# Kernel tuning notes

Measured on AMD Instinct MI355X. Metric: run time of the kernel, lower is better.

## Reference

```python
import jax, jax.numpy as jnp
import numpy as np

B = 16384   # batch (agents x parallel envs)
IN = 12     # input_dim
H = 64      # hidden_dim -> 2H = 128
OUT = 25    # output_dim (forced by x[:,0:5]..x[:,20:25] slicing)


def setup_inputs() -> dict:
    key = jax.random.key(0)
    ks = jax.random.split(key, 24)
    n = lambda k, s: jax.random.normal(k, s, dtype=jnp.float32)
    s = 0.1  # scale params to keep SiLU/softmax in a sane range
    return {
        "x": n(ks[0], (B, IN)),
        "na": 4,
        # mlp_in: Linear(IN, 2H) + SiLU
        "W_in": n(ks[1], (2 * H, IN)) * s, "b_in": n(ks[2], (2 * H,)) * s,
        # first attention (2H)
        "Aq4": n(ks[3], (2 * H, 2 * H)) * s, "Bq4": n(ks[4], (2 * H,)) * s,
        "Ak4": n(ks[5], (2 * H, 2 * H)) * s, "Bk4": n(ks[6], (2 * H,)) * s,
        "Av4": n(ks[7], (2 * H, 2 * H)) * s, "Bv4": n(ks[8], (2 * H,)) * s,
        # mlp_hidden_4: Linear(2H, H) + SiLU
        "W_h": n(ks[9], (H, 2 * H)) * s, "b_h": n(ks[10], (H,)) * s,
        # second attention (H)
        "Aq7": n(ks[11], (H, H)) * s, "Bq7": n(ks[12], (H,)) * s,
        "Ak7": n(ks[13], (H, H)) * s, "Bk7": n(ks[14], (H,)) * s,
        "Av7": n(ks[15], (H, H)) * s, "Bv7": n(ks[16], (H,)) * s,
        # mlp_out: Linear(H, OUT) + SiLU
        "W_out": n(ks[17], (OUT, H)) * s, "b_out": n(ks[18], (OUT,)) * s,
    }


def _attn(h, Aq, Bq, Ak, Bk, Av, Bv):
    # h: [B, D]; torch does bmm(A, x^T)+B with x of shape [B,1,D] -> seq-len-1
    # attention, i.e. scores are an outer product q k^T of shape [B, D, D].
    q = jax.nn.silu(h @ Aq.T + Bq)                      # [B, D]
    k = jax.nn.silu(h @ Ak.T + Bk)                      # [B, D]
    v = jax.nn.silu(h @ Av.T + Bv)                      # [B, D]
    a = jax.nn.softmax(q[:, :, None] * k[:, None, :], axis=2)  # [B, D, D]
    return jax.nn.silu(jnp.einsum("bij,bj->bi", a, v))  # [B, D]


def reference(x, na, W_in, b_in, Aq4, Bq4, Ak4, Bk4, Av4, Bv4,
              W_h, b_h, Aq7, Bq7, Ak7, Bk7, Av7, Bv7, W_out, b_out):
    h = jax.nn.silu(x @ W_in.T + b_in)                  # [B, 2H]
    h = _attn(h, Aq4, Bq4, Ak4, Bk4, Av4, Bv4)          # [B, 2H]
    h = jax.nn.silu(h @ W_h.T + b_h)                    # [B, H]
    h = _attn(h, Aq7, Bq7, Ak7, Bk7, Av7, Bv7)          # [B, H]
    y = jax.nn.silu(h @ W_out.T + b_out)                # [B, 25]

    # block-diagonal quadratic-form assembly (l=2, kron with ones(1,2))
    M11 = jnp.sum(y[:, 0:5] ** 2, axis=1)               # [B]
    M12 = jnp.sum(y[:, 5:10] ** 2, axis=1)
    M21 = jnp.sum(y[:, 10:15] ** 2, axis=1)
    M22 = jnp.sum(y[:, 15:20] ** 2, axis=1)
    Mpp = jnp.sum(y[:, 20:25] ** 2, axis=1)             # [B]
    q = y[:, :4]                                        # [B, 4] = [q0,q1,q2,q3]
    # M = [[diag(M11), diag(M12)],[diag(M21), diag(M22)]] (each 2x2 diag)
    quad = (M11 * (q[:, 0] ** 2 + q[:, 1] ** 2)
            + (M12 + M21) * (q[:, 0] * q[:, 2] + q[:, 1] * q[:, 3])
            + M22 * (q[:, 2] ** 2 + q[:, 3] ** 2))
    return (quad + Mpp)[:, None]                        # [B, 1]
```

## Files before the change

kernel.cpp:

```cpp
#include <hip/hip_runtime.h>

#define RPW 4
#define WAVES 4
#define RPB (RPW * WAVES)
#define NM 14

using short8 = __attribute__((ext_vector_type(8))) short;
using f32x4  = __attribute__((ext_vector_type(4))) float;

#define LOG2E 1.4426950408889634f

static __device__ __forceinline__ float ex2(float x) { return __builtin_amdgcn_exp2f(x); }
static __device__ __forceinline__ float rcpf_(float x) { return __builtin_amdgcn_rcpf(x); }
static __device__ __forceinline__ float silu_(float x) {
    return x * rcpf_(1.0f + ex2(-x * LOG2E));
}
static __device__ __forceinline__ unsigned short bfhi(float x) {
    return (unsigned short)(__float_as_uint(x) >> 16);
}
static __device__ __forceinline__ unsigned short bfrn(float x) {
    unsigned u = __float_as_uint(x);
    return (unsigned short)((u + 0x7fffu + ((u >> 16) & 1u)) >> 16);
}
static __device__ __forceinline__ float bf2f(unsigned short h) {
    return __uint_as_float(((unsigned)h) << 16);
}

template <int CTRL>
static __device__ __forceinline__ float dpp_rot(float v) {
    return __uint_as_float(
        __builtin_amdgcn_update_dpp(0u, __float_as_uint(v), CTRL, 0xF, 0xF, true));
}
static __device__ __forceinline__ float rsum16(float v) {
    v += dpp_rot<0x128>(v);
    v += dpp_rot<0x124>(v);
    v += dpp_rot<0x122>(v);
    v += dpp_rot<0x121>(v);
    return v;
}

__constant__ float c_invfact[15] = {
    1.f, 1.f, 0.5f, 1.f/6, 1.f/24, 1.f/120, 1.f/720, 1.f/5040, 1.f/40320,
    1.f/362880, 1.f/3628800, 1.f/39916800, 1.f/479001600,
    1.f/6227020800.f, 1.f/87178291200.f};

template <int O, int I>
__device__ __forceinline__ void tr(const float* __restrict__ s, float* __restrict__ d,
                                   int t0, int stride) {
    for (int idx = t0; idx < O * I; idx += stride) {
        int o = idx / I, in = idx - o * I;
        d[in * O + o] = s[idx];
    }
}

template <int TILES, int KTS, int K>
__device__ __forceinline__ void frag_cvt(const float* __restrict__ A,
                                         unsigned short* __restrict__ dst,
                                         int t0, int stride) {
    const int total = TILES * KTS * 2 * 512;
    for (int idx = t0; idx < total; idx += stride) {
        int e = idx & 7;
        int lane = (idx >> 3) & 63;
        int h = (idx >> 9) & 1;
        int kt = (idx >> 10) % KTS;
        int tile = (idx >> 10) / KTS;
        int row = tile * 16 + (lane & 15);
        int col = kt * 32 + (lane >> 4) * 8 + e;
        float a = A[row * K + col];
        unsigned short hi = bfhi(a);
        dst[idx] = h ? bfhi(a - bf2f(hi)) : hi;
    }
}

__global__ void tweights(const float* __restrict__ s0, const float* __restrict__ s1,
                         const float* __restrict__ s2, const float* __restrict__ s3,
                         const float* __restrict__ s4, const float* __restrict__ s5,
                         const float* __restrict__ s6, const float* __restrict__ s7,
                         float* __restrict__ ws) {
    const int stride = gridDim.x * blockDim.x;
    const int t0 = blockIdx.x * blockDim.x + threadIdx.x;
    tr<128, 12>(s0, ws + 0, t0, stride);
    unsigned short* u4 = (unsigned short*)(ws + 1536);
    frag_cvt<8, 4, 128>(s1, u4 + 0,     t0, stride);
    frag_cvt<8, 4, 128>(s2, u4 + 32768, t0, stride);
    frag_cvt<8, 4, 128>(s3, u4 + 65536, t0, stride);
    unsigned short* wh = (unsigned short*)(ws + 50688);
    frag_cvt<4, 4, 128>(s4, wh, t0, stride);
    unsigned short* u7 = (unsigned short*)(ws + 58880);
    frag_cvt<4, 2, 64>(s5, u7 + 0,     t0, stride);
    frag_cvt<4, 2, 64>(s6, u7 + 8192,  t0, stride);
    frag_cvt<4, 2, 64>(s7, u7 + 16384, t0, stride);
}

__global__ __launch_bounds__(256, 4) void fused_net(
    const float* __restrict__ x, const float* __restrict__ ws,
    const float* __restrict__ b_in,
    const float* __restrict__ Bq4, const float* __restrict__ Bk4, const float* __restrict__ Bv4,
    const float* __restrict__ b_h,
    const float* __restrict__ Bq7, const float* __restrict__ Bk7, const float* __restrict__ Bv7,
    const float* __restrict__ Wout, const float* __restrict__ b_out,
    float* __restrict__ out) {
    __shared__ __align__(16) unsigned short hAhi[16][136], hAlo[16][136];
    __shared__ __align__(16) unsigned short h2hi[16][80],  h2lo[16][80];
    __shared__ __align__(16) float sQ[16][132];
    __shared__ __align__(16) unsigned short sKVb[16][132][2];
    __shared__ __align__(16) float h3T[WAVES][64][RPW];
    __shared__ __align__(16) float sXT[WAVES][12][RPW];
    __shared__ __align__(16) float sY[WAVES][RPW][26];

    const int tid = threadIdx.x;
    const int w = tid >> 6;
    const int l = tid & 63;
    const int row0 = blockIdx.x * RPB + w * RPW;
    const int m16 = l & 15, quad = l >> 4;
    const int g = l & 15, r = l >> 4;
    const int R = w * RPW + r;

    const float* WinT = ws + 0;

    float bias4[6];
    #pragma unroll
    for (int t = 0; t < 6; t++) {
        const int nt = w * 6 + t;
        const int mat = nt >> 3;
        const int n = (nt & 7) * 16 + m16;
        const float* bp = (mat == 0) ? Bq4 : (mat == 1) ? Bk4 : Bv4;
        bias4[t] = bp[n];
    }
    float biasH = b_h[w * 16 + m16];
    float bias7[3];
    #pragma unroll
    for (int t = 0; t < 3; t++) {
        const int nt = w * 3 + t;
        const int mat = nt >> 2;
        const int n = (nt & 3) * 16 + m16;
        const float* bp = (mat == 0) ? Bq7 : (mat == 1) ? Bk7 : Bv7;
        bias7[t] = bp[n];
    }

    if (l < 12 * RPW) {
        float v = x[row0 * 12 + l];
        int rr = l / 12, in = l - rr * 12;
        sXT[w][in][rr] = v;
    }

    {
        float2 bb = *(const float2*)&b_in[2 * l];
        float a0[RPW], a1[RPW];
        #pragma unroll
        for (int rr = 0; rr < RPW; rr++) { a0[rr] = bb.x; a1[rr] = bb.y; }
        #pragma unroll
        for (int in = 0; in < 12; in++) {
            float2 wv = *(const float2*)&WinT[in * 128 + 2 * l];
            float4 xr = *(const float4*)&sXT[w][in][0];
            a0[0] = fmaf(xr.x, wv.x, a0[0]); a1[0] = fmaf(xr.x, wv.y, a1[0]);
            a0[1] = fmaf(xr.y, wv.x, a0[1]); a1[1] = fmaf(xr.y, wv.y, a1[1]);
            a0[2] = fmaf(xr.z, wv.x, a0[2]); a1[2] = fmaf(xr.z, wv.y, a1[2]);
            a0[3] = fmaf(xr.w, wv.x, a0[3]); a1[3] = fmaf(xr.w, wv.y, a1[3]);
        }
        #pragma unroll
        for (int rr = 0; rr < RPW; rr++) {
            float h0 = silu_(a0[rr]), h1 = silu_(a1[rr]);
            unsigned short h0h = bfhi(h0), h1h = bfhi(h1);
            float r0 = h0 - bf2f(h0h), r1 = h1 - bf2f(h1h);
            *(unsigned*)&hAhi[w * 4 + rr][2 * l] = (unsigned)h0h | ((unsigned)h1h << 16);
            *(unsigned*)&hAlo[w * 4 + rr][2 * l] = (unsigned)bfhi(r0) | ((unsigned)bfhi(r1) << 16);
        }
    }
    __syncthreads();

    {
        short8 Ah[4], Al[4];
        #pragma unroll
        for (int kt = 0; kt < 4; kt++) {
            Ah[kt] = *(const short8*)&hAhi[m16][kt * 32 + quad * 8];
            Al[kt] = *(const short8*)&hAlo[m16][kt * 32 + quad * 8];
        }
        const unsigned short* F4 = (const unsigned short*)(ws + 1536);
        short8 cb[4][2], nb[4][2];
        auto ldt = [&](int t, short8 fr[4][2]) {
            const int nt = w * 6 + t;
            const int mat = nt >> 3, tile = nt & 7;
            const unsigned short* bp = F4 + mat * 32768 + tile * 4096 + l * 8;
            #pragma unroll
            for (int kt = 0; kt < 4; kt++) {
                fr[kt][0] = *(const short8*)(bp + kt * 1024);
                fr[kt][1] = *(const short8*)(bp + kt * 1024 + 512);
            }
        };
        ldt(0, cb);
        #pragma unroll
        for (int t = 0; t < 6; t++) {
            if (t < 5) ldt(t + 1, nb);
            f32x4 acc0 = {0.f, 0.f, 0.f, 0.f};
            f32x4 acc1 = {0.f, 0.f, 0.f, 0.f};
            #pragma unroll
            for (int kt = 0; kt < 4; kt++) {
                acc0 = __builtin_amdgcn_mfma_f32_16x16x32_bf16(Ah[kt], cb[kt][0], acc0, 0, 0, 0);
                acc1 = __builtin_amdgcn_mfma_f32_16x16x32_bf16(Ah[kt], cb[kt][1], acc1, 0, 0, 0);
                acc1 = __builtin_amdgcn_mfma_f32_16x16x32_bf16(Al[kt], cb[kt][0], acc1, 0, 0, 0);
            }
            const int nt = w * 6 + t;
            const int mat = nt >> 3;
            const int n = (nt & 7) * 16 + m16;
            const float b = bias4[t];
            #pragma unroll
            for (int reg = 0; reg < 4; reg++) {
                int row = quad * 4 + reg;
                float val = silu_(b + acc0[reg] + acc1[reg]);
                if (mat == 0)      sQ[row][n] = val;
                else if (mat == 1) sKVb[row][n][0] = bfrn(val);
                else               sKVb[row][n][1] = bfrn(val);
            }
            #pragma unroll
            for (int kt = 0; kt < 4; kt++) { cb[kt][0] = nb[kt][0]; cb[kt][1] = nb[kt][1]; }
        }
    }
    __syncthreads();

    short8 whf[4][2];
    {
        const unsigned short* bp = (const unsigned short*)(ws + 50688) + w * 4096 + l * 8;
        #pragma unroll
        for (int kt = 0; kt < 4; kt++) {
            whf[kt][0] = *(const short8*)(bp + kt * 1024);
            whf[kt][1] = *(const short8*)(bp + kt * 1024 + 512);
        }
    }
    {
        float dmom[NM];
        float nmom[NM + 1];
        #pragma unroll
        for (int m = 0; m < NM; m++) dmom[m] = 0.f;
        #pragma unroll
        for (int m = 0; m <= NM; m++) nmom[m] = 0.f;
        uint4 u0 = *(const uint4*)&sKVb[R][g * 8][0];
        uint4 u1 = *(const uint4*)&sKVb[R][g * 8 + 4][0];
        unsigned us[8] = {u0.x, u0.y, u0.z, u0.w, u1.x, u1.y, u1.z, u1.w};
        #pragma unroll
        for (int jj = 0; jj < 8; jj++) {
            unsigned u = us[jj];
            float kf = __uint_as_float(u << 16);
            float vf = __uint_as_float(u & 0xffff0000u);
            nmom[0] += vf;
            float p = kf;
            dmom[0] += p; nmom[1] = fmaf(vf, p, nmom[1]);
            #pragma unroll
            for (int m = 1; m < NM; m++) {
                p *= kf;
                dmom[m] += p;
                nmom[m + 1] = fmaf(vf, p, nmom[m + 1]);
            }
        }
        #pragma unroll
        for (int m = 0; m < NM; m++) dmom[m] = rsum16(dmom[m]);
        #pragma unroll
        for (int m = 0; m <= NM; m++) nmom[m] = rsum16(nmom[m]);
        float cd[NM + 1], cn[NM + 1];
        cd[0] = 128.f; cn[0] = nmom[0];
        #pragma unroll
        for (int m = 1; m <= NM; m++) {
            cd[m] = dmom[m - 1] * c_invfact[m];
            cn[m] = nmom[m] * c_invfact[m];
        }
        float4 qa = *(const float4*)&sQ[R][g * 8];
        float4 qb = *(const float4*)&sQ[R][g * 8 + 4];
        float qs[8] = {qa.x, qa.y, qa.z, qa.w, qb.x, qb.y, qb.z, qb.w};
        unsigned hiw[4], low[4];
        #pragma unroll
        for (int i = 0; i < 8; i++) {
            float t = qs[i];
            float d = cd[NM], nn = cn[NM];
            #pragma unroll
            for (int m = NM - 1; m >= 0; m--) {
                d = fmaf(d, t, cd[m]);
                nn = fmaf(nn, t, cn[m]);
            }
            float o = silu_(nn * rcpf_(d));
            unsigned short oh = bfhi(o);
            unsigned short olo = bfhi(o - bf2f(oh));
            if (i & 1) { hiw[i >> 1] |= ((unsigned)oh) << 16; low[i >> 1] |= ((unsigned)olo) << 16; }
            else       { hiw[i >> 1] = oh; low[i >> 1] = olo; }
        }
        *(uint4*)&hAhi[R][g * 8] = make_uint4(hiw[0], hiw[1], hiw[2], hiw[3]);
        *(uint4*)&hAlo[R][g * 8] = make_uint4(low[0], low[1], low[2], low[3]);
    }
    __syncthreads();

    short8 u7f[3][2][2];
    {
        const unsigned short* U7 = (const unsigned short*)(ws + 58880);
        #pragma unroll
        for (int t = 0; t < 3; t++) {
            const int nt = w * 3 + t;
            const int mat = nt >> 2, tile = nt & 3;
            const unsigned short* bp = U7 + mat * 8192 + tile * 2048 + l * 8;
            #pragma unroll
            for (int kt = 0; kt < 2; kt++) {
                u7f[t][kt][0] = *(const short8*)(bp + kt * 1024);
                u7f[t][kt][1] = *(const short8*)(bp + kt * 1024 + 512);
            }
        }
    }
    {
        short8 Ah[4], Al[4];
        #pragma unroll
        for (int kt = 0; kt < 4; kt++) {
            Ah[kt] = *(const short8*)&hAhi[m16][kt * 32 + quad * 8];
            Al[kt] = *(const short8*)&hAlo[m16][kt * 32 + quad * 8];
        }
        const int n = w * 16 + m16;
        f32x4 acc0 = {0.f, 0.f, 0.f, 0.f};
        f32x4 acc1 = {0.f, 0.f, 0.f, 0.f};
        #pragma unroll
        for (int kt = 0; kt < 4; kt++) {
            acc0 = __builtin_amdgcn_mfma_f32_16x16x32_bf16(Ah[kt], whf[kt][0], acc0, 0, 0, 0);
            acc1 = __builtin_amdgcn_mfma_f32_16x16x32_bf16(Ah[kt], whf[kt][1], acc1, 0, 0, 0);
            acc1 = __builtin_amdgcn_mfma_f32_16x16x32_bf16(Al[kt], whf[kt][0], acc1, 0, 0, 0);
        }
        #pragma unroll
        for (int reg = 0; reg < 4; reg++) {
            int row = quad * 4 + reg;
            float hv = silu_(biasH + acc0[reg] + acc1[reg]);
            unsigned short hh = bfhi(hv);
            h2hi[row][n] = hh;
            h2lo[row][n] = bfhi(hv - bf2f(hh));
        }
    }
    __syncthreads();

    {
        short8 Ah[2], Al[2];
        #pragma unroll
        for (int kt = 0; kt < 2; kt++) {
            Ah[kt] = *(const short8*)&h2hi[m16][kt * 32 + quad * 8];
            Al[kt] = *(const short8*)&h2lo[m16][kt * 32 + quad * 8];
        }
        #pragma unroll
        for (int t = 0; t < 3; t++) {
            const int nt = w * 3 + t;
            const int mat = nt >> 2;
            const int n = (nt & 3) * 16 + m16;
            f32x4 acc0 = {0.f, 0.f, 0.f, 0.f};
            f32x4 acc1 = {0.f, 0.f, 0.f, 0.f};
            #pragma unroll
            for (int kt = 0; kt < 2; kt++) {
                acc0 = __builtin_amdgcn_mfma_f32_16x16x32_bf16(Ah[kt], u7f[t][kt][0], acc0, 0, 0, 0);
                acc1 = __builtin_amdgcn_mfma_f32_16x16x32_bf16(Ah[kt], u7f[t][kt][1], acc1, 0, 0, 0);
                acc1 = __builtin_amdgcn_mfma_f32_16x16x32_bf16(Al[kt], u7f[t][kt][0], acc1, 0, 0, 0);
            }
            const float b = bias7[t];
            #pragma unroll
            for (int reg = 0; reg < 4; reg++) {
                int row = quad * 4 + reg;
                float val = silu_(b + acc0[reg] + acc1[reg]);
                if (mat == 0)      sQ[row][n] = val;
                else if (mat == 1) sKVb[row][n][0] = bfrn(val);
                else               sKVb[row][n][1] = bfrn(val);
            }
        }
    }
    __syncthreads();

    float4 wq[8];
    float bb7;
    {
        const int o_ = l & 31;
        const int half_ = l >> 5;
        const int oc_ = (o_ < 25) ? o_ : 0;
        const float* wp = Wout + oc_ * 64 + half_ * 32;
        #pragma unroll
        for (int q = 0; q < 8; q++) wq[q] = *(const float4*)&wp[4 * q];
        bb7 = (half_ == 0) ? b_out[oc_] : 0.f;
    }
    {
        float dmom[NM];
        float nmom[NM + 1];
        #pragma unroll
        for (int m = 0; m < NM; m++) dmom[m] = 0.f;
        #pragma unroll
        for (int m = 0; m <= NM; m++) nmom[m] = 0.f;
        uint2 u0 = *(const uint2*)&sKVb[R][g * 4][0];
        uint2 u1 = *(const uint2*)&sKVb[R][g * 4 + 2][0];
        unsigned us[4] = {u0.x, u0.y, u1.x, u1.y};
        #pragma unroll
        for (int jj = 0; jj < 4; jj++) {
            unsigned u = us[jj];
            float kf = __uint_as_float(u << 16);
            float vf = __uint_as_float(u & 0xffff0000u);
            nmom[0] += vf;
            float p = kf;
            dmom[0] += p; nmom[1] = fmaf(vf, p, nmom[1]);
            #pragma unroll
            for (int m = 1; m < NM; m++) {
                p *= kf;
                dmom[m] += p;
                nmom[m + 1] = fmaf(vf, p, nmom[m + 1]);
            }
        }
        #pragma unroll
        for (int m = 0; m < NM; m++) dmom[m] = rsum16(dmom[m]);
        #pragma unroll
        for (int m = 0; m <= NM; m++) nmom[m] = rsum16(nmom[m]);
        float cd[NM + 1], cn[NM + 1];
        cd[0] = 64.f; cn[0] = nmom[0];
        #pragma unroll
        for (int m = 1; m <= NM; m++) {
            cd[m] = dmom[m - 1] * c_invfact[m];
            cn[m] = nmom[m] * c_invfact[m];
        }
        float4 qa = *(const float4*)&sQ[R][g * 4];
        float qs[4] = {qa.x, qa.y, qa.z, qa.w};
        #pragma unroll
        for (int i = 0; i < 4; i++) {
            float t = qs[i];
            float d = cd[NM], nn = cn[NM];
            #pragma unroll
            for (int m = NM - 1; m >= 0; m--) {
                d = fmaf(d, t, cd[m]);
                nn = fmaf(nn, t, cn[m]);
            }
            h3T[w][g * 4 + i][r] = silu_(nn * rcpf_(d));
        }
    }

    {
        const int half = l >> 5;
        float y[RPW];
        #pragma unroll
        for (int rr = 0; rr < RPW; rr++) y[rr] = bb7;
        const int in0 = half * 32;
        #pragma unroll
        for (int q = 0; q < 8; q++) {
            float wa[4] = {wq[q].x, wq[q].y, wq[q].z, wq[q].w};
            #pragma unroll
            for (int ii = 0; ii < 4; ii++) {
                int in = in0 + 4 * q + ii;
                float4 xr = *(const float4*)&h3T[w][in][0];
                y[0] = fmaf(xr.x, wa[ii], y[0]);
                y[1] = fmaf(xr.y, wa[ii], y[1]);
                y[2] = fmaf(xr.z, wa[ii], y[2]);
                y[3] = fmaf(xr.w, wa[ii], y[3]);
            }
        }
        #pragma unroll
        for (int rr = 0; rr < RPW; rr++) {
            float full = y[rr] + __shfl_xor(y[rr], 32, 64);
            if (l < 25) sY[w][rr][l] = silu_(full);
        }
    }

    if (l < RPW) {
        const int rr = l;
        float y[25];
        #pragma unroll
        for (int c = 0; c < 25; c++) y[c] = sY[w][rr][c];
        float M11 = 0.f, M12 = 0.f, M21 = 0.f, M22 = 0.f, Mpp = 0.f;
        #pragma unroll
        for (int c = 0; c < 5; c++) {
            M11 = fmaf(y[c], y[c], M11);
            M12 = fmaf(y[5 + c], y[5 + c], M12);
            M21 = fmaf(y[10 + c], y[10 + c], M21);
            M22 = fmaf(y[15 + c], y[15 + c], M22);
            Mpp = fmaf(y[20 + c], y[20 + c], Mpp);
        }
        float quad = M11 * (y[0] * y[0] + y[1] * y[1])
                   + (M12 + M21) * (y[0] * y[2] + y[1] * y[3])
                   + M22 * (y[2] * y[2] + y[3] * y[3]);
        out[row0 + rr] = quad + Mpp;
    }
}

extern "C" void kernel_launch(void* const* d_in, const int* in_sizes, int n_in,
                              void* d_out, int out_size, void* d_ws, size_t ws_size,
                              hipStream_t stream) {
    const float* x    = (const float*)d_in[0];
    const float* W_in = (const float*)d_in[2];
    const float* b_in = (const float*)d_in[3];
    const float* Aq4  = (const float*)d_in[4];
    const float* Bq4  = (const float*)d_in[5];
    const float* Ak4  = (const float*)d_in[6];
    const float* Bk4  = (const float*)d_in[7];
    const float* Av4  = (const float*)d_in[8];
    const float* Bv4  = (const float*)d_in[9];
    const float* W_h  = (const float*)d_in[10];
    const float* b_h  = (const float*)d_in[11];
    const float* Aq7  = (const float*)d_in[12];
    const float* Bq7  = (const float*)d_in[13];
    const float* Ak7  = (const float*)d_in[14];
    const float* Bk7  = (const float*)d_in[15];
    const float* Av7  = (const float*)d_in[16];
    const float* Bv7  = (const float*)d_in[17];
    const float* Wout = (const float*)d_in[18];
    const float* bout = (const float*)d_in[19];
    float* ws = (float*)d_ws;

    tweights<<<256, 256, 0, stream>>>(W_in, Aq4, Ak4, Av4, W_h, Aq7, Ak7, Av7, ws);

    const int B = in_sizes[0] / 12;
    const int grid = B / RPB;
    fused_net<<<grid, 256, 0, stream>>>(x, ws, b_in, Bq4, Bk4, Bv4,
                                        b_h, Bq7, Bk7, Bv7, Wout, bout, (float*)d_out);
}
```

Before: 132.6 us.

## Split block into two 8-row half-batches and interleave MFMA and moment phases

Each 16-row block is split into two independent 8-row sub-batches (A and B) with separate shared buffers. The schedule is software-pipelined so one sub-batch's MFMA projections run interleaved with the other's VALU-heavy Taylor-moment softmax and epilogue, using 32-lane reductions. The aim is to overlap matrix-core work with vector ALU work inside a wave. In exchange, each MFMA now uses only 8 of its 16 rows, doubling MFMA issue per row, and shared memory use and register pressure go up.

```diff
diff --git a/kernel.cpp b/kernel.cpp
--- a/kernel.cpp
+++ b/kernel.cpp
@@ -1,8 +1,6 @@
 #include <hip/hip_runtime.h>
 
-#define RPW 4
-#define WAVES 4
-#define RPB (RPW * WAVES)
+#define RPB 16
 #define NM 14
 
 using short8 = __attribute__((ext_vector_type(8))) short;
@@ -38,6 +36,12 @@
     v += dpp_rot<0x121>(v);
     return v;
 }
+static __device__ __forceinline__ float rsum32(float v) {
+    v = rsum16(v);
+    v += __uint_as_float(
+        (unsigned)__builtin_amdgcn_ds_swizzle((int)__float_as_uint(v), 0x401F));
+    return v;
+}
 
 __constant__ float c_invfact[15] = {
     1.f, 1.f, 0.5f, 1.f/6, 1.f/24, 1.f/120, 1.f/720, 1.f/5040, 1.f/40320,
@@ -52,7 +56,6 @@
         d[in * O + o] = s[idx];
     }
 }
-
 template <int TILES, int KTS, int K>
 __device__ __forceinline__ void frag_cvt(const float* __restrict__ A,
                                          unsigned short* __restrict__ dst,
@@ -92,6 +95,288 @@
     frag_cvt<4, 2, 64>(s7, u7 + 16384, t0, stride);
 }
 
+
+#define STAGE_X(S, OFF) \
+    if (l < 24) { \
+        float v = x[(base + (OFF) + w * 2) * 12 + l]; \
+        int rr = l / 12, in = l - rr * 12; \
+        sXT##S[w][in][rr] = v; \
+    }
+
+#define PH1(S) { \
+    float2 bb = *(const float2*)&b_in[2 * l]; \
+    float a0[2], a1[2]; \
+    a0[0] = bb.x; a0[1] = bb.x; a1[0] = bb.y; a1[1] = bb.y; \
+    _Pragma("unroll") \
+    for (int in = 0; in < 12; in++) { \
+        float2 wv = *(const float2*)&WinT[in * 128 + 2 * l]; \
+        float2 xr = *(const float2*)&sXT##S[w][in][0]; \
+        a0[0] = fmaf(xr.x, wv.x, a0[0]); a1[0] = fmaf(xr.x, wv.y, a1[0]); \
+        a0[1] = fmaf(xr.y, wv.x, a0[1]); a1[1] = fmaf(xr.y, wv.y, a1[1]); \
+    } \
+    _Pragma("unroll") \
+    for (int rr = 0; rr < 2; rr++) { \
+        float h0 = silu_(a0[rr]), h1 = silu_(a1[rr]); \
+        unsigned short h0h = bfhi(h0), h1h = bfhi(h1); \
+        float r0 = h0 - bf2f(h0h), r1 = h1 - bf2f(h1h); \
+        *(unsigned*)&hAhi##S[w * 2 + rr][2 * l] = (unsigned)h0h | ((unsigned)h1h << 16); \
+        *(unsigned*)&hAlo##S[w * 2 + rr][2 * l] = (unsigned)bfhi(r0) | ((unsigned)bfhi(r1) << 16); \
+    } }
+
+#define LDA4(S) \
+    short8 Ah##S[4], Al##S[4]; \
+    _Pragma("unroll") \
+    for (int kt = 0; kt < 4; kt++) { \
+        Ah##S[kt] = *(const short8*)&hAhi##S[m8][kt * 32 + quad * 8]; \
+        Al##S[kt] = *(const short8*)&hAlo##S[m8][kt * 32 + quad * 8]; \
+    }
+
+#define TILE4(S, T) { \
+    const int nt = w * 6 + (T); \
+    const int mat = nt >> 3; \
+    const int n = (nt & 7) * 16 + m16; \
+    const unsigned short* bp = F4 + mat * 32768 + (nt & 7) * 4096 + l * 8; \
+    f32x4 acc0 = {0.f, 0.f, 0.f, 0.f}; \
+    f32x4 acc1 = {0.f, 0.f, 0.f, 0.f}; \
+    _Pragma("unroll") \
+    for (int kt = 0; kt < 4; kt++) { \
+        short8 bh = *(const short8*)(bp + kt * 1024); \
+        short8 bl = *(const short8*)(bp + kt * 1024 + 512); \
+        acc0 = __builtin_amdgcn_mfma_f32_16x16x32_bf16(Ah##S[kt], bh, acc0, 0, 0, 0); \
+        acc1 = __builtin_amdgcn_mfma_f32_16x16x32_bf16(Ah##S[kt], bl, acc1, 0, 0, 0); \
+        acc1 = __builtin_amdgcn_mfma_f32_16x16x32_bf16(Al##S[kt], bh, acc1, 0, 0, 0); \
+    } \
+    const float bv = bias4[(T)]; \
+    if (quad < 2) { \
+        _Pragma("unroll") \
+        for (int reg = 0; reg < 4; reg++) { \
+            int row = quad * 4 + reg; \
+            float val = silu_(bv + acc0[reg] + acc1[reg]); \
+            if (mat == 0)      sQ##S[row][n] = val; \
+            else if (mat == 1) sKV##S[row][n][0] = bfrn(val); \
+            else               sKV##S[row][n][1] = bfrn(val); \
+        } \
+    } }
+
+#define P3_STATE(S) \
+    const int row3 = w * 2 + r32; \
+    uint4 u3 = *(const uint4*)&sKV##S[row3][g32 * 4][0]; \
+    float dm[NM], nm[NM + 1];
+
+#define P3_MOM(S) { \
+    _Pragma("unroll") for (int m = 0; m < NM; m++) dm[m] = 0.f; \
+    _Pragma("unroll") for (int m = 0; m <= NM; m++) nm[m] = 0.f; \
+    unsigned usv[4] = {u3.x, u3.y, u3.z, u3.w}; \
+    _Pragma("unroll") \
+    for (int jj = 0; jj < 4; jj++) { \
+        unsigned u = usv[jj]; \
+        float kf = __uint_as_float(u << 16); \
+        float vf = __uint_as_float(u & 0xffff0000u); \
+        nm[0] += vf; \
+        float p = kf; \
+        dm[0] += p; nm[1] = fmaf(vf, p, nm[1]); \
+        _Pragma("unroll") \
+        for (int m = 1; m < NM; m++) { \
+            p *= kf; \
+            dm[m] += p; \
+            nm[m + 1] = fmaf(vf, p, nm[m + 1]); \
+        } \
+    } }
+
+#define P3_REDD() \
+    _Pragma("unroll") for (int m = 0; m < NM; m++) dm[m] = rsum32(dm[m]);
+#define P3_REDN() \
+    _Pragma("unroll") for (int m = 0; m <= NM; m++) nm[m] = rsum32(nm[m]);
+
+#define P3_HORN(S) { \
+    float cd[NM + 1], cn[NM + 1]; \
+    cd[0] = 128.f; cn[0] = nm[0]; \
+    _Pragma("unroll") \
+    for (int m = 1; m <= NM; m++) { \
+        cd[m] = dm[m - 1] * c_invfact[m]; \
+        cn[m] = nm[m] * c_invfact[m]; \
+    } \
+    float4 qa = *(const float4*)&sQ##S[row3][g32 * 4]; \
+    float qs[4] = {qa.x, qa.y, qa.z, qa.w}; \
+    unsigned hiw[2], low[2]; \
+    _Pragma("unroll") \
+    for (int i = 0; i < 4; i++) { \
+        float t = qs[i]; \
+        float d = cd[NM], nn = cn[NM]; \
+        _Pragma("unroll") \
+        for (int m = NM - 1; m >= 0; m--) { \
+            d = fmaf(d, t, cd[m]); \
+            nn = fmaf(nn, t, cn[m]); \
+        } \
+        float o = silu_(nn * rcpf_(d)); \
+        unsigned short oh = bfhi(o); \
+        unsigned short olo = bfhi(o - bf2f(oh)); \
+        if (i & 1) { hiw[i >> 1] |= ((unsigned)oh) << 16; low[i >> 1] |= ((unsigned)olo) << 16; } \
+        else       { hiw[i >> 1] = oh; low[i >> 1] = olo; } \
+    } \
+    *(uint2*)&hAhi##S[row3][g32 * 4] = make_uint2(hiw[0], hiw[1]); \
+    *(uint2*)&hAlo##S[row3][g32 * 4] = make_uint2(low[0], low[1]); }
+
+#define P4_MFMA(S) \
+    short8 Ah4[4], Al4[4]; \
+    _Pragma("unroll") \
+    for (int kt = 0; kt < 4; kt++) { \
+        Ah4[kt] = *(const short8*)&hAhi##S[m8][kt * 32 + quad * 8]; \
+        Al4[kt] = *(const short8*)&hAlo##S[m8][kt * 32 + quad * 8]; \
+    } \
+    const unsigned short* bp4 = WH + w * 4096 + l * 8; \
+    f32x4 p40 = {0.f, 0.f, 0.f, 0.f}; \
+    f32x4 p41 = {0.f, 0.f, 0.f, 0.f}; \
+    _Pragma("unroll") \
+    for (int kt = 0; kt < 4; kt++) { \
+        short8 bh = *(const short8*)(bp4 + kt * 1024); \
+        short8 bl = *(const short8*)(bp4 + kt * 1024 + 512); \
+        p40 = __builtin_amdgcn_mfma_f32_16x16x32_bf16(Ah4[kt], bh, p40, 0, 0, 0); \
+        p41 = __builtin_amdgcn_mfma_f32_16x16x32_bf16(Ah4[kt], bl, p41, 0, 0, 0); \
+        p41 = __builtin_amdgcn_mfma_f32_16x16x32_bf16(Al4[kt], bh, p41, 0, 0, 0); \
+    }
+
+#define P4_EPI(S) { \
+    const int n4 = w * 16 + m16; \
+    if (quad < 2) { \
+        _Pragma("unroll") \
+        for (int reg = 0; reg < 4; reg++) { \
+            int row = quad * 4 + reg; \
+            float hv = silu_(biasH + p40[reg] + p41[reg]); \
+            unsigned short hh = bfhi(hv); \
+            h2hi##S[row][n4] = hh; \
+            h2lo##S[row][n4] = bfhi(hv - bf2f(hh)); \
+        } \
+    } }
+
+#define LDA2(S) \
+    short8 Ah2##S[2], Al2##S[2]; \
+    _Pragma("unroll") \
+    for (int kt = 0; kt < 2; kt++) { \
+        Ah2##S[kt] = *(const short8*)&h2hi##S[m8][kt * 32 + quad * 8]; \
+        Al2##S[kt] = *(const short8*)&h2lo##S[m8][kt * 32 + quad * 8]; \
+    }
+
+#define TILE7(S, T) { \
+    const int nt = w * 3 + (T); \
+    const int mat = nt >> 2; \
+    const int n = (nt & 3) * 16 + m16; \
+    const unsigned short* bp = U7 + mat * 8192 + (nt & 3) * 2048 + l * 8; \
+    f32x4 acc0 = {0.f, 0.f, 0.f, 0.f}; \
+    f32x4 acc1 = {0.f, 0.f, 0.f, 0.f}; \
+    _Pragma("unroll") \
+    for (int kt = 0; kt < 2; kt++) { \
+        short8 bh = *(const short8*)(bp + kt * 1024); \
+        short8 bl = *(const short8*)(bp + kt * 1024 + 512); \
+        acc0 = __builtin_amdgcn_mfma_f32_16x16x32_bf16(Ah2##S[kt], bh, acc0, 0, 0, 0); \
+        acc1 = __builtin_amdgcn_mfma_f32_16x16x32_bf16(Ah2##S[kt], bl, acc1, 0, 0, 0); \
+        acc1 = __builtin_amdgcn_mfma_f32_16x16x32_bf16(Al2##S[kt], bh, acc1, 0, 0, 0); \
+    } \
+    const float bv = bias7[(T)]; \
+    if (quad < 2) { \
+        _Pragma("unroll") \
+        for (int reg = 0; reg < 4; reg++) { \
+            int row = quad * 4 + reg; \
+            float val = silu_(bv + acc0[reg] + acc1[reg]); \
+            if (mat == 0)      sQ##S[row][n] = val; \
+            else if (mat == 1) sKV##S[row][n][0] = bfrn(val); \
+            else               sKV##S[row][n][1] = bfrn(val); \
+        } \
+    } }
+
+#define P6_STATE(S) \
+    const int row6 = w * 2 + r32; \
+    uint2 u6 = *(const uint2*)&sKV##S[row6][g32 * 2][0]; \
+    float dm6[NM], nm6[NM + 1];
+
+#define P6_MOM(S) { \
+    _Pragma("unroll") for (int m = 0; m < NM; m++) dm6[m] = 0.f; \
+    _Pragma("unroll") for (int m = 0; m <= NM; m++) nm6[m] = 0.f; \
+    unsigned usv[2] = {u6.x, u6.y}; \
+    _Pragma("unroll") \
+    for (int jj = 0; jj < 2; jj++) { \
+        unsigned u = usv[jj]; \
+        float kf = __uint_as_float(u << 16); \
+        float vf = __uint_as_float(u & 0xffff0000u); \
+        nm6[0] += vf; \
+        float p = kf; \
+        dm6[0] += p; nm6[1] = fmaf(vf, p, nm6[1]); \
+        _Pragma("unroll") \
+        for (int m = 1; m < NM; m++) { \
+            p *= kf; \
+            dm6[m] += p; \
+            nm6[m + 1] = fmaf(vf, p, nm6[m + 1]); \
+        } \
+    } }
+
+#define P6_RED() \
+    _Pragma("unroll") for (int m = 0; m < NM; m++) dm6[m] = rsum32(dm6[m]); \
+    _Pragma("unroll") for (int m = 0; m <= NM; m++) nm6[m] = rsum32(nm6[m]);
+
+#define P6_HORN(S) { \
+    float cd[NM + 1], cn[NM + 1]; \
+    cd[0] = 64.f; cn[0] = nm6[0]; \
+    _Pragma("unroll") \
+    for (int m = 1; m <= NM; m++) { \
+        cd[m] = dm6[m - 1] * c_invfact[m]; \
+        cn[m] = nm6[m] * c_invfact[m]; \
+    } \
+    float2 qa = *(const float2*)&sQ##S[row6][g32 * 2]; \
+    float qs[2] = {qa.x, qa.y}; \
+    _Pragma("unroll") \
+    for (int i = 0; i < 2; i++) { \
+        float t = qs[i]; \
+        float d = cd[NM], nn = cn[NM]; \
+        _Pragma("unroll") \
+        for (int m = NM - 1; m >= 0; m--) { \
+            d = fmaf(d, t, cd[m]); \
+            nn = fmaf(nn, t, cn[m]); \
+        } \
+        h3T##S[w][g32 * 2 + i][r32] = silu_(nn * rcpf_(d)); \
+    } }
+
+#define P7(S) { \
+    const int o_ = l & 31; \
+    const int half_ = l >> 5; \
+    const int oc_ = (o_ < 25) ? o_ : 0; \
+    float bb7 = (half_ == 0) ? b_out[oc_] : 0.f; \
+    float y0 = bb7, y1 = bb7; \
+    const int in0 = half_ * 32; \
+    const float* wp = Wout + oc_ * 64 + in0; \
+    _Pragma("unroll") \
+    for (int q8 = 0; q8 < 8; q8++) { \
+        float4 wq4 = *(const float4*)&wp[4 * q8]; \
+        float wa[4] = {wq4.x, wq4.y, wq4.z, wq4.w}; \
+        _Pragma("unroll") \
+        for (int ii = 0; ii < 4; ii++) { \
+            float2 xr = *(const float2*)&h3T##S[w][in0 + 4 * q8 + ii][0]; \
+            y0 = fmaf(xr.x, wa[ii], y0); \
+            y1 = fmaf(xr.y, wa[ii], y1); \
+        } \
+    } \
+    float f0 = y0 + __shfl_xor(y0, 32, 64); \
+    float f1 = y1 + __shfl_xor(y1, 32, 64); \
+    if (l < 25) { sY##S[w][0][l] = silu_(f0); sY##S[w][1][l] = silu_(f1); } }
+
+#define P8(S, OFF) \
+    if (l < 2) { \
+        float yv[25]; \
+        _Pragma("unroll") for (int c = 0; c < 25; c++) yv[c] = sY##S[w][l][c]; \
+        float M11 = 0.f, M12 = 0.f, M21 = 0.f, M22 = 0.f, Mpp = 0.f; \
+        _Pragma("unroll") \
+        for (int c = 0; c < 5; c++) { \
+            M11 = fmaf(yv[c], yv[c], M11); \
+            M12 = fmaf(yv[5 + c], yv[5 + c], M12); \
+            M21 = fmaf(yv[10 + c], yv[10 + c], M21); \
+            M22 = fmaf(yv[15 + c], yv[15 + c], M22); \
+            Mpp = fmaf(yv[20 + c], yv[20 + c], Mpp); \
+        } \
+        float qf = M11 * (yv[0] * yv[0] + yv[1] * yv[1]) \
+                 + (M12 + M21) * (yv[0] * yv[2] + yv[1] * yv[3]) \
+                 + M22 * (yv[2] * yv[2] + yv[3] * yv[3]); \
+        out[base + (OFF) + w * 2 + l] = qf + Mpp; \
+    }
+
 __global__ __launch_bounds__(256, 4) void fused_net(
     const float* __restrict__ x, const float* __restrict__ ws,
     const float* __restrict__ b_in,
@@ -100,23 +385,28 @@
     const float* __restrict__ Bq7, const float* __restrict__ Bk7, const float* __restrict__ Bv7,
     const float* __restrict__ Wout, const float* __restrict__ b_out,
     float* __restrict__ out) {
-    __shared__ __align__(16) unsigned short hAhi[16][136], hAlo[16][136];
-    __shared__ __align__(16) unsigned short h2hi[16][80],  h2lo[16][80];
-    __shared__ __align__(16) float sQ[16][132];
-    __shared__ __align__(16) unsigned short sKVb[16][132][2];
-    __shared__ __align__(16) float h3T[WAVES][64][RPW];
-    __shared__ __align__(16) float sXT[WAVES][12][RPW];
-    __shared__ __align__(16) float sY[WAVES][RPW][26];
+    __shared__ __align__(16) unsigned short hAhiA[8][136], hAloA[8][136];
+    __shared__ __align__(16) unsigned short hAhiB[8][136], hAloB[8][136];
+    __shared__ __align__(16) unsigned short h2hiA[8][80],  h2loA[8][80];
+    __shared__ __align__(16) unsigned short h2hiB[8][80],  h2loB[8][80];
+    __shared__ __align__(16) float sQA[8][132], sQB[8][132];
+    __shared__ __align__(16) unsigned short sKVA[8][132][2], sKVB[8][132][2];
+    __shared__ __align__(16) float h3TA[4][64][2], h3TB[4][64][2];
+    __shared__ __align__(16) float sXTA[4][12][2], sXTB[4][12][2];
+    __shared__ __align__(16) float sYA[4][2][26], sYB[4][2][26];
 
     const int tid = threadIdx.x;
     const int w = tid >> 6;
     const int l = tid & 63;
-    const int row0 = blockIdx.x * RPB + w * RPW;
+    const int base = blockIdx.x * RPB;
     const int m16 = l & 15, quad = l >> 4;
-    const int g = l & 15, r = l >> 4;
-    const int R = w * RPW + r;
+    const int m8 = m16 & 7;
+    const int g32 = l & 31, r32 = l >> 5;
 
     const float* WinT = ws + 0;
+    const unsigned short* F4 = (const unsigned short*)(ws + 1536);
+    const unsigned short* WH = (const unsigned short*)(ws + 50688);
+    const unsigned short* U7 = (const unsigned short*)(ws + 58880);
 
     float bias4[6];
     #pragma unroll
@@ -138,337 +428,83 @@
         bias7[t] = bp[n];
     }
 
-    if (l < 12 * RPW) {
-        float v = x[row0 * 12 + l];
-        int rr = l / 12, in = l - rr * 12;
-        sXT[w][in][rr] = v;
-    }
+    STAGE_X(A, 0)
+    STAGE_X(B, 8)
+    PH1(A)
+    __syncthreads();
 
     {
-        float2 bb = *(const float2*)&b_in[2 * l];
-        float a0[RPW], a1[RPW];
-        #pragma unroll
-        for (int rr = 0; rr < RPW; rr++) { a0[rr] = bb.x; a1[rr] = bb.y; }
-        #pragma unroll
-        for (int in = 0; in < 12; in++) {
-            float2 wv = *(const float2*)&WinT[in * 128 + 2 * l];
-            float4 xr = *(const float4*)&sXT[w][in][0];
-            a0[0] = fmaf(xr.x, wv.x, a0[0]); a1[0] = fmaf(xr.x, wv.y, a1[0]);
-            a0[1] = fmaf(xr.y, wv.x, a0[1]); a1[1] = fmaf(xr.y, wv.y, a1[1]);
-            a0[2] = fmaf(xr.z, wv.x, a0[2]); a1[2] = fmaf(xr.z, wv.y, a1[2]);
-            a0[3] = fmaf(xr.w, wv.x, a0[3]); a1[3] = fmaf(xr.w, wv.y, a1[3]);
-        }
-        #pragma unroll
-        for (int rr = 0; rr < RPW; rr++) {
-            float h0 = silu_(a0[rr]), h1 = silu_(a1[rr]);
-            unsigned short h0h = bfhi(h0), h1h = bfhi(h1);
-            float r0 = h0 - bf2f(h0h), r1 = h1 - bf2f(h1h);
-            *(unsigned*)&hAhi[w * 4 + rr][2 * l] = (unsigned)h0h | ((unsigned)h1h << 16);
-            *(unsigned*)&hAlo[w * 4 + rr][2 * l] = (unsigned)bfhi(r0) | ((unsigned)bfhi(r1) << 16);
-        }
+        LDA4(A)
+        TILE4(A, 0)
+        PH1(B)
+        TILE4(A, 1)
+        TILE4(A, 2)
+        TILE4(A, 3)
+        TILE4(A, 4)
+        TILE4(A, 5)
     }
     __syncthreads();
 
     {
-        short8 Ah[4], Al[4];
-        #pragma unroll
-        for (int kt = 0; kt < 4; kt++) {
-            Ah[kt] = *(const short8*)&hAhi[m16][kt * 32 + quad * 8];
-            Al[kt] = *(const short8*)&hAlo[m16][kt * 32 + quad * 8];
-        }
-        const unsigned short* F4 = (const unsigned short*)(ws + 1536);
-        short8 cb[4][2], nb[4][2];
-        auto ldt = [&](int t, short8 fr[4][2]) {
-            const int nt = w * 6 + t;
-            const int mat = nt >> 3, tile = nt & 7;
-            const unsigned short* bp = F4 + mat * 32768 + tile * 4096 + l * 8;
-            #pragma unroll
-            for (int kt = 0; kt < 4; kt++) {
-                fr[kt][0] = *(const short8*)(bp + kt * 1024);
-                fr[kt][1] = *(const short8*)(bp + kt * 1024 + 512);
-            }
-        };
-        ldt(0, cb);
-        #pragma unroll
-        for (int t = 0; t < 6; t++) {
-            if (t < 5) ldt(t + 1, nb);
-            f32x4 acc0 = {0.f, 0.f, 0.f, 0.f};
-            f32x4 acc1 = {0.f, 0.f, 0.f, 0.f};
-            #pragma unroll
-            for (int kt = 0; kt < 4; kt++) {
-                acc0 = __builtin_amdgcn_mfma_f32_16x16x32_bf16(Ah[kt], cb[kt][0], acc0, 0, 0, 0);
-                acc1 = __builtin_amdgcn_mfma_f32_16x16x32_bf16(Ah[kt], cb[kt][1], acc1, 0, 0, 0);
-                acc1 = __builtin_amdgcn_mfma_f32_16x16x32_bf16(Al[kt], cb[kt][0], acc1, 0, 0, 0);
-            }
-            const int nt = w * 6 + t;
-            const int mat = nt >> 3;
-            const int n = (nt & 7) * 16 + m16;
-            const float b = bias4[t];
-            #pragma unroll
-            for (int reg = 0; reg < 4; reg++) {
-                int row = quad * 4 + reg;
-                float val = silu_(b + acc0[reg] + acc1[reg]);
-                if (mat == 0)      sQ[row][n] = val;
-                else if (mat == 1) sKVb[row][n][0] = bfrn(val);
-                else               sKVb[row][n][1] = bfrn(val);
-            }
-            #pragma unroll
-            for (int kt = 0; kt < 4; kt++) { cb[kt][0] = nb[kt][0]; cb[kt][1] = nb[kt][1]; }
-        }
+        LDA4(B)
+        P3_STATE(A)
+        TILE4(B, 0)
+        P3_MOM(A)
+        TILE4(B, 1)
+        TILE4(B, 2)
+        P3_REDD()
+        TILE4(B, 3)
+        P3_REDN()
+        TILE4(B, 4)
+        P3_HORN(A)
+        TILE4(B, 5)
     }
     __syncthreads();
 
-    short8 whf[4][2];
     {
-        const unsigned short* bp = (const unsigned short*)(ws + 50688) + w * 4096 + l * 8;
-        #pragma unroll
-        for (int kt = 0; kt < 4; kt++) {
-            whf[kt][0] = *(const short8*)(bp + kt * 1024);
-            whf[kt][1] = *(const short8*)(bp + kt * 1024 + 512);
-        }
-    }
+        P4_MFMA(A)
+        P3_STATE(B)
+        P3_MOM(B)
+        P4_EPI(A)
+        P3_REDD()
+        P3_REDN()
+        P3_HORN(B)
+    }
+    __syncthreads();
+
     {
-        float dmom[NM];
-        float nmom[NM + 1];
-        #pragma unroll
-        for (int m = 0; m < NM; m++) dmom[m] = 0.f;
-        #pragma unroll
-        for (int m = 0; m <= NM; m++) nmom[m] = 0.f;
-        uint4 u0 = *(const uint4*)&sKVb[R][g * 8][0];
-        uint4 u1 = *(const uint4*)&sKVb[R][g * 8 + 4][0];
-        unsigned us[8] = {u0.x, u0.y, u0.z, u0.w, u1.x, u1.y, u1.z, u1.w};
-        #pragma unroll
-        for (int jj = 0; jj < 8; jj++) {
-            unsigned u = us[jj];
-            float kf = __uint_as_float(u << 16);
-            float vf = __uint_as_float(u & 0xffff0000u);
-            nmom[0] += vf;
-            float p = kf;
-            dmom[0] += p; nmom[1] = fmaf(vf, p, nmom[1]);
-            #pragma unroll
-            for (int m = 1; m < NM; m++) {
-                p *= kf;
-                dmom[m] += p;
-                nmom[m + 1] = fmaf(vf, p, nmom[m + 1]);
-            }
-        }
-        #pragma unroll
-        for (int m = 0; m < NM; m++) dmom[m] = rsum16(dmom[m]);
-        #pragma unroll
-        for (int m = 0; m <= NM; m++) nmom[m] = rsum16(nmom[m]);
-        float cd[NM + 1], cn[NM + 1];
-        cd[0] = 128.f; cn[0] = nmom[0];
-        #pragma unroll
-        for (int m = 1; m <= NM; m++) {
-            cd[m] = dmom[m - 1] * c_invfact[m];
-            cn[m] = nmom[m] * c_invfact[m];
-        }
-        float4 qa = *(const float4*)&sQ[R][g * 8];
-        float4 qb = *(const float4*)&sQ[R][g * 8 + 4];
-        float qs[8] = {qa.x, qa.y, qa.z, qa.w, qb.x, qb.y, qb.z, qb.w};
-        unsigned hiw[4], low[4];
-        #pragma unroll
-        for (int i = 0; i < 8; i++) {
-            float t = qs[i];
-            float d = cd[NM], nn = cn[NM];
-            #pragma unroll
-            for (int m = NM - 1; m >= 0; m--) {
-                d = fmaf(d, t, cd[m]);
-                nn = fmaf(nn, t, cn[m]);
-            }
-            float o = silu_(nn * rcpf_(d));
-            unsigned short oh = bfhi(o);
-            unsigned short olo = bfhi(o - bf2f(oh));
-            if (i & 1) { hiw[i >> 1] |= ((unsigned)oh) << 16; low[i >> 1] |= ((unsigned)olo) << 16; }
-            else       { hiw[i >> 1] = oh; low[i >> 1] = olo; }
-        }
-        *(uint4*)&hAhi[R][g * 8] = make_uint4(hiw[0], hiw[1], hiw[2], hiw[3]);
-        *(uint4*)&hAlo[R][g * 8] = make_uint4(low[0], low[1], low[2], low[3]);
+        LDA2(A)
+        TILE7(A, 0)
+        P4_MFMA(B)
+        TILE7(A, 1)
+        TILE7(A, 2)
+        P4_EPI(B)
     }
     __syncthreads();
 
-    short8 u7f[3][2][2];
     {
-        const unsigned short* U7 = (const unsigned short*)(ws + 58880);
-        #pragma unroll
-        for (int t = 0; t < 3; t++) {
-            const int nt = w * 3 + t;
-            const int mat = nt >> 2, tile = nt & 3;
-            const unsigned short* bp = U7 + mat * 8192 + tile * 2048 + l * 8;
-            #pragma unroll
-            for (int kt = 0; kt < 2; kt++) {
-                u7f[t][kt][0] = *(const short8*)(bp + kt * 1024);
-                u7f[t][kt][1] = *(const short8*)(bp + kt * 1024 + 512);
-            }
-        }
-    }
+        LDA2(B)
+        P6_STATE(A)
+        TILE7(B, 0)
+        P6_MOM(A)
+        TILE7(B, 1)
+        P6_RED()
+        TILE7(B, 2)
+        P6_HORN(A)
+    }
+    __syncthreads();
+
     {
-        short8 Ah[4], Al[4];
-        #pragma unroll
-        for (int kt = 0; kt < 4; kt++) {
-            Ah[kt] = *(const short8*)&hAhi[m16][kt * 32 + quad * 8];
-            Al[kt] = *(const short8*)&hAlo[m16][kt * 32 + quad * 8];
-        }
-        const int n = w * 16 + m16;
-        f32x4 acc0 = {0.f, 0.f, 0.f, 0.f};
-        f32x4 acc1 = {0.f, 0.f, 0.f, 0.f};
-        #pragma unroll
-        for (int kt = 0; kt < 4; kt++) {
-            acc0 = __builtin_amdgcn_mfma_f32_16x16x32_bf16(Ah[kt], whf[kt][0], acc0, 0, 0, 0);
-            acc1 = __builtin_amdgcn_mfma_f32_16x16x32_bf16(Ah[kt], whf[kt][1], acc1, 0, 0, 0);
-            acc1 = __builtin_amdgcn_mfma_f32_16x16x32_bf16(Al[kt], whf[kt][0], acc1, 0, 0, 0);
-        }
-        #pragma unroll
-        for (int reg = 0; reg < 4; reg++) {
-            int row = quad * 4 + reg;
-            float hv = silu_(biasH + acc0[reg] + acc1[reg]);
-            unsigned short hh = bfhi(hv);
-            h2hi[row][n] = hh;
-            h2lo[row][n] = bfhi(hv - bf2f(hh));
-        }
-    }
-    __syncthreads();
-
-    {
-        short8 Ah[2], Al[2];
-        #pragma unroll
-        for (int kt = 0; kt < 2; kt++) {
-            Ah[kt] = *(const short8*)&h2hi[m16][kt * 32 + quad * 8];
-            Al[kt] = *(const short8*)&h2lo[m16][kt * 32 + quad * 8];
-        }
-        #pragma unroll
-        for (int t = 0; t < 3; t++) {
-            const int nt = w * 3 + t;
-            const int mat = nt >> 2;
-            const int n = (nt & 3) * 16 + m16;
-            f32x4 acc0 = {0.f, 0.f, 0.f, 0.f};
-            f32x4 acc1 = {0.f, 0.f, 0.f, 0.f};
-            #pragma unroll
-            for (int kt = 0; kt < 2; kt++) {
-                acc0 = __builtin_amdgcn_mfma_f32_16x16x32_bf16(Ah[kt], u7f[t][kt][0], acc0, 0, 0, 0);
-                acc1 = __builtin_amdgcn_mfma_f32_16x16x32_bf16(Ah[kt], u7f[t][kt][1], acc1, 0, 0, 0);
-                acc1 = __builtin_amdgcn_mfma_f32_16x16x32_bf16(Al[kt], u7f[t][kt][0], acc1, 0, 0, 0);
-            }
-            const float b = bias7[t];
-            #pragma unroll
-            for (int reg = 0; reg < 4; reg++) {
-                int row = quad * 4 + reg;
-                float val = silu_(b + acc0[reg] + acc1[reg]);
-                if (mat == 0)      sQ[row][n] = val;
-                else if (mat == 1) sKVb[row][n][0] = bfrn(val);
-                else               sKVb[row][n][1] = bfrn(val);
-            }
-        }
-    }
-    __syncthreads();
-
-    float4 wq[8];
-    float bb7;
-    {
-        const int o_ = l & 31;
-        const int half_ = l >> 5;
-        const int oc_ = (o_ < 25) ? o_ : 0;
-        const float* wp = Wout + oc_ * 64 + half_ * 32;
-        #pragma unroll
-        for (int q = 0; q < 8; q++) wq[q] = *(const float4*)&wp[4 * q];
-        bb7 = (half_ == 0) ? b_out[oc_] : 0.f;
-    }
-    {
-        float dmom[NM];
-        float nmom[NM + 1];
-        #pragma unroll
-        for (int m = 0; m < NM; m++) dmom[m] = 0.f;
-        #pragma unroll
-        for (int m = 0; m <= NM; m++) nmom[m] = 0.f;
-        uint2 u0 = *(const uint2*)&sKVb[R][g * 4][0];
-        uint2 u1 = *(const uint2*)&sKVb[R][g * 4 + 2][0];
-        unsigned us[4] = {u0.x, u0.y, u1.x, u1.y};
-        #pragma unroll
-        for (int jj = 0; jj < 4; jj++) {
-            unsigned u = us[jj];
-            float kf = __uint_as_float(u << 16);
-            float vf = __uint_as_float(u & 0xffff0000u);
-            nmom[0] += vf;
-            float p = kf;
-            dmom[0] += p; nmom[1] = fmaf(vf, p, nmom[1]);
-            #pragma unroll
-            for (int m = 1; m < NM; m++) {
-                p *= kf;
-                dmom[m] += p;
-                nmom[m + 1] = fmaf(vf, p, nmom[m + 1]);
-            }
-        }
-        #pragma unroll
-        for (int m = 0; m < NM; m++) dmom[m] = rsum16(dmom[m]);
-        #pragma unroll
-        for (int m = 0; m <= NM; m++) nmom[m] = rsum16(nmom[m]);
-        float cd[NM + 1], cn[NM + 1];
-        cd[0] = 64.f; cn[0] = nmom[0];
-        #pragma unroll
-        for (int m = 1; m <= NM; m++) {
-            cd[m] = dmom[m - 1] * c_invfact[m];
-            cn[m] = nmom[m] * c_invfact[m];
-        }
-        float4 qa = *(const float4*)&sQ[R][g * 4];
-        float qs[4] = {qa.x, qa.y, qa.z, qa.w};
-        #pragma unroll
-        for (int i = 0; i < 4; i++) {
-            float t = qs[i];
-            float d = cd[NM], nn = cn[NM];
-            #pragma unroll
-            for (int m = NM - 1; m >= 0; m--) {
-                d = fmaf(d, t, cd[m]);
-                nn = fmaf(nn, t, cn[m]);
-            }
-            h3T[w][g * 4 + i][r] = silu_(nn * rcpf_(d));
-        }
-    }
-
-    {
-        const int half = l >> 5;
-        float y[RPW];
-        #pragma unroll
-        for (int rr = 0; rr < RPW; rr++) y[rr] = bb7;
-        const int in0 = half * 32;
-        #pragma unroll
-        for (int q = 0; q < 8; q++) {
-            float wa[4] = {wq[q].x, wq[q].y, wq[q].z, wq[q].w};
-            #pragma unroll
-            for (int ii = 0; ii < 4; ii++) {
-                int in = in0 + 4 * q + ii;
-                float4 xr = *(const float4*)&h3T[w][in][0];
-                y[0] = fmaf(xr.x, wa[ii], y[0]);
-                y[1] = fmaf(xr.y, wa[ii], y[1]);
-                y[2] = fmaf(xr.z, wa[ii], y[2]);
-                y[3] = fmaf(xr.w, wa[ii], y[3]);
-            }
-        }
-        #pragma unroll
-        for (int rr = 0; rr < RPW; rr++) {
-            float full = y[rr] + __shfl_xor(y[rr], 32, 64);
-            if (l < 25) sY[w][rr][l] = silu_(full);
-        }
-    }
-
-    if (l < RPW) {
-        const int rr = l;
-        float y[25];
-        #pragma unroll
-        for (int c = 0; c < 25; c++) y[c] = sY[w][rr][c];
-        float M11 = 0.f, M12 = 0.f, M21 = 0.f, M22 = 0.f, Mpp = 0.f;
-        #pragma unroll
-        for (int c = 0; c < 5; c++) {
-            M11 = fmaf(y[c], y[c], M11);
-            M12 = fmaf(y[5 + c], y[5 + c], M12);
-            M21 = fmaf(y[10 + c], y[10 + c], M21);
-            M22 = fmaf(y[15 + c], y[15 + c], M22);
-            Mpp = fmaf(y[20 + c], y[20 + c], Mpp);
-        }
-        float quad = M11 * (y[0] * y[0] + y[1] * y[1])
-                   + (M12 + M21) * (y[0] * y[2] + y[1] * y[3])
-                   + M22 * (y[2] * y[2] + y[3] * y[3]);
-        out[row0 + rr] = quad + Mpp;
-    }
+        P6_STATE(B)
+        P6_MOM(B)
+        P7(A)
+        P6_RED()
+        P8(A, 0)
+        P6_HORN(B)
+    }
+
+    P7(B)
+    P8(B, 8)
 }
 
 extern "C" void kernel_launch(void* const* d_in, const int* in_sizes, int n_in,
```

Measured after the change: 163.3 us. 1.23x slower.
